# Performance work log

Measured on AMD Instinct MI355X. Metric: run time of the kernel, lower is better.

The kernel has to match this reference:

```python
import jax, jax.numpy as jnp
import numpy as np

B, T, C, H = 2, 2048, 1024, 16
HD = C // H  # 64


def setup_inputs() -> dict:
    key = jax.random.key(0)
    ks = jax.random.split(key, 5)
    x = jax.random.normal(ks[0], (B, T, C), jnp.float32)
    scale = 0.02
    Wq = jax.random.normal(ks[1], (C, C), jnp.float32) * scale
    Wk = jax.random.normal(ks[2], (C, C), jnp.float32) * scale
    Wv = jax.random.normal(ks[3], (C, C), jnp.float32) * scale
    Wo = jax.random.normal(ks[4], (C, C), jnp.float32) * scale
    # RoPE tables: freqs_cis = exp(i * pos * theta_j), theta_j = 10000^(-2j/HD)
    pos = jnp.arange(T, dtype=jnp.float32)
    theta = 10000.0 ** (-jnp.arange(0, HD, 2, dtype=jnp.float32) / HD)  # [HD/2]
    ang = pos[:, None] * theta[None, :]  # [T, HD/2]
    cos = jnp.cos(ang)
    sin = jnp.sin(ang)
    return {"x": x, "Wq": Wq, "Wk": Wk, "Wv": Wv, "Wo": Wo, "cos": cos, "sin": sin}


def _rope(t, cos, sin):
    # t: [B,T,H,HD]; pairs (even, odd) along last dim form complex numbers
    b, s, h, hd = t.shape
    tr = t.reshape(b, s, h, hd // 2, 2)
    t0, t1 = tr[..., 0], tr[..., 1]
    c = cos[None, :, None, :]  # [1,T,1,HD/2]
    sn = sin[None, :, None, :]
    o0 = t0 * c - t1 * sn
    o1 = t0 * sn + t1 * c
    return jnp.stack([o0, o1], axis=-1).reshape(b, s, h, hd)


def reference(x, Wq, Wk, Wv, Wo, cos, sin):
    b, t, c = x.shape
    h, hd = H, c // H
    q = (x @ Wq.T).reshape(b, t, h, hd)
    k = (x @ Wk.T).reshape(b, t, h, hd)
    v = (x @ Wv.T).reshape(b, t, h, hd)
    q = _rope(q, cos, sin)
    k = _rope(k, cos, sin)
    # explicit causal attention with full TxT score matrix (as in source)
    att = jnp.einsum("bthd,bshd->bhts", q, k) / jnp.sqrt(jnp.float32(hd))
    causal = jnp.tril(jnp.ones((t, t), dtype=bool))
    att = jnp.where(causal[None, None, :, :], att, -jnp.inf)
    att = jax.nn.softmax(att, axis=-1)
    out = jnp.einsum("bhts,bshd->bthd", att, v).reshape(b, t, c)
    return out @ Wo.T
```

## Files before the change

### kernel.cpp

```cpp
#include <hip/hip_runtime.h>
#include <cstdint>
#include <cstddef>


typedef __bf16 bf16;
typedef float  f32x4  __attribute__((ext_vector_type(4)));
typedef __bf16 bf16x4 __attribute__((ext_vector_type(4)));
typedef __bf16 bf16x8 __attribute__((ext_vector_type(8)));

constexpr int Bb = 2, Tt = 2048, Cc = 1024, Hh = 16;
constexpr int Mrows = Bb * Tt;
constexpr int NT = Tt / 64;
constexpr int LDS_ = 72;

#define GLOAD_LDS16(gp, lp)                                                      \
    __builtin_amdgcn_global_load_lds(                                            \
        (const __attribute__((address_space(1))) void*)(gp),                     \
        (__attribute__((address_space(3))) void*)(lp), 16, 0, 0)

#define QUAD_T(v0, v1, v2, v3, c2)                                               \
    {                                                                            \
        float e0 = (c2 & 1) ? v0 : v1, e1 = (c2 & 1) ? v2 : v3;                  \
        e0 = __shfl_xor(e0, 1); e1 = __shfl_xor(e1, 1);                          \
        if (c2 & 1) { v0 = e0; v2 = e1; } else { v1 = e0; v3 = e1; }             \
        float f0 = (c2 & 2) ? v0 : v2, f1 = (c2 & 2) ? v1 : v3;                  \
        f0 = __shfl_xor(f0, 2); f1 = __shfl_xor(f1, 2);                          \
        if (c2 & 2) { v0 = f0; v1 = f1; } else { v2 = f0; v3 = f1; }             \
    }

__global__ __launch_bounds__(256) void convert_k(const float* __restrict__ x,
                                                 const float* __restrict__ Wq,
                                                 const float* __restrict__ Wk,
                                                 const float* __restrict__ Wv,
                                                 const float* __restrict__ Wo,
                                                 const float* __restrict__ cosb,
                                                 const float* __restrict__ sinb,
                                                 bf16* __restrict__ xb,
                                                 bf16* __restrict__ Wqkv,
                                                 bf16* __restrict__ Wob,
                                                 float2* __restrict__ cs)
{
    if (blockIdx.x >= 4096) {
        int pi = ((blockIdx.x - 4096) * 256 + threadIdx.x) * 8;
#pragma unroll
        for (int u = 0; u < 8; ++u)
            cs[pi + u] = float2{cosb[pi + u], sinb[pi + u]};
        return;
    }
    uint32_t id = blockIdx.x * 256 + threadIdx.x;
    const float* src; bf16* dst; float sc = 1.0f;
    if (id < 524288u) {
        uint32_t tile = id >> 10, slot = id & 1023;
        uint32_t row = (tile >> 4) * 128 + (slot >> 9) * 64 +
                       ((slot >> 6) & 3) * 16 + (slot & 15);
        uint32_t k = (tile & 15) * 64 + ((slot >> 8) & 1) * 32 + ((slot >> 4) & 3) * 8;
        src = x + (size_t)row * 1024 + k;
        dst = xb + (size_t)id * 8;
    } else if (id < 917504u) {
        uint32_t t2 = id - 524288u;
        uint32_t tile = t2 >> 10, slot = t2 & 1023;
        uint32_t n = (tile >> 4) * 128 + (slot >> 9) * 64 +
                     ((slot >> 6) & 3) * 16 + (slot & 15);
        uint32_t k = (tile & 15) * 64 + ((slot >> 8) & 1) * 32 + ((slot >> 4) & 3) * 8;
        if (n < 1024)      { src = Wq + (size_t)n * 1024 + k;
                             sc = 0.125f * 1.44269504088896f; }
        else if (n < 2048)   src = Wk + (size_t)(n - 1024) * 1024 + k;
        else                 src = Wv + (size_t)(n - 2048) * 1024 + k;
        dst = Wqkv + (size_t)t2 * 8;
    } else {
        uint32_t t3 = id - 917504u;
        uint32_t tile = t3 >> 9, slot = t3 & 511;
        uint32_t n = (tile >> 4) * 64 + (slot >> 8) * 32 +
                     ((slot >> 6) & 1) * 16 + (slot & 15);
        uint32_t k = (tile & 15) * 64 + ((slot >> 7) & 1) * 32 + ((slot >> 4) & 3) * 8;
        src = Wo + (size_t)n * 1024 + k;
        dst = Wob + (size_t)t3 * 8;
    }
    float4 v0 = *(const float4*)(src);
    float4 v1 = *(const float4*)(src + 4);
    bf16x8 t;
    t[0] = (bf16)(v0.x*sc); t[1] = (bf16)(v0.y*sc); t[2] = (bf16)(v0.z*sc); t[3] = (bf16)(v0.w*sc);
    t[4] = (bf16)(v1.x*sc); t[5] = (bf16)(v1.y*sc); t[6] = (bf16)(v1.z*sc); t[7] = (bf16)(v1.w*sc);
    *(bf16x8*)dst = t;
}

__global__ __launch_bounds__(256) void gemm_qkv(const bf16* __restrict__ A,
                                                const bf16* __restrict__ W,
                                                bf16* __restrict__ QK,
                                                bf16* __restrict__ Vt,
                                                const float2* __restrict__ cs)
{
    __shared__ bf16 As[8192];
    __shared__ bf16 Ws[8192];
    const int tid  = threadIdx.x;
    const int lane = tid & 63, wave = tid >> 6;
    const int rhw = wave >> 1, chw = wave & 1;
    const int wr = rhw * 64, wc = chw * 64;
    const int l16 = lane & 15, lq = lane >> 4;
    const int row0 = blockIdx.x * 128, col0 = blockIdx.y * 128;

    f32x4 acc[4][4];
#pragma unroll
    for (int i = 0; i < 4; ++i)
#pragma unroll
        for (int j = 0; j < 4; ++j) acc[i][j] = f32x4{0.f, 0.f, 0.f, 0.f};

    const bf16* At = A + (size_t)blockIdx.x * 16 * 8192;
    const bf16* Wt = W + (size_t)blockIdx.y * 16 * 8192;

    for (int kb = 0; kb < 16; ++kb) {
        const bf16* at = At + kb * 8192;
        const bf16* wt = Wt + kb * 8192;
#pragma unroll
        for (int rnd = 0; rnd < 4; ++rnd) {
            const int seg = rnd * 4 + wave;
            GLOAD_LDS16(at + seg * 512 + lane * 8, &As[seg * 512]);
            GLOAD_LDS16(wt + seg * 512 + lane * 8, &Ws[seg * 512]);
        }
        __syncthreads();
#pragma unroll
        for (int ks = 0; ks < 2; ++ks) {
            bf16x8 af[4], bfr[4];
#pragma unroll
            for (int i = 0; i < 4; ++i)
                af[i] = *(const bf16x8*)(&As[(rhw * 512 + ks * 256 + i * 64 + lq * 16 + l16) * 8]);
#pragma unroll
            for (int j = 0; j < 4; ++j)
                bfr[j] = *(const bf16x8*)(&Ws[(chw * 512 + ks * 256 + j * 64 + lq * 16 + l16) * 8]);
#pragma unroll
            for (int i = 0; i < 4; ++i)
#pragma unroll
                for (int j = 0; j < 4; ++j)
                    acc[i][j] = __builtin_amdgcn_mfma_f32_16x16x32_bf16(
                        af[i], bfr[j], acc[i][j], 0, 0, 0);
        }
        __syncthreads();
    }

    const int c2 = l16 & 3, g4 = (l16 >> 2) * 4;
    if (blockIdx.y < 16) {
#pragma unroll
        for (int i = 0; i < 4; ++i)
#pragma unroll
            for (int j = 0; j < 4; ++j) {
                float v0 = acc[i][j][0], v1 = acc[i][j][1];
                float v2 = acc[i][j][2], v3 = acc[i][j][3];
                QUAD_T(v0, v1, v2, v3, c2);
                const int row = row0 + wr + i * 16 + lq * 4 + c2;
                const int t   = row & (Tt - 1);
                const int colb = wc + j * 16 + g4;
                const int p0   = (colb & 63) >> 1;
                float4 cp = *(const float4*)(&cs[t * 32 + p0]);
                bf16x4 pk;
                pk[0] = (bf16)(v0 * cp.x - v1 * cp.y);
                pk[1] = (bf16)(v0 * cp.y + v1 * cp.x);
                pk[2] = (bf16)(v2 * cp.z - v3 * cp.w);
                pk[3] = (bf16)(v2 * cp.w + v3 * cp.z);
                *(bf16x4*)(&QK[(size_t)row * 2048 + col0 + colb]) = pk;
            }
    } else {
#pragma unroll
        for (int i = 0; i < 4; ++i)
#pragma unroll
            for (int j = 0; j < 4; ++j) {
                const int dfull = col0 - 2048 + wc + j * 16 + l16;
                const int h = dfull >> 6, d = dfull & 63;
                const int row = row0 + wr + i * 16 + lq * 4;
                const int b = row >> 11, t = row & (Tt - 1);
                bf16x4 pk;
                pk[0] = (bf16)acc[i][j][0]; pk[1] = (bf16)acc[i][j][1];
                pk[2] = (bf16)acc[i][j][2]; pk[3] = (bf16)acc[i][j][3];
                *(bf16x4*)(&Vt[((size_t)(b * 16 + h) * 64 + d) * (size_t)Tt + t]) = pk;
            }
    }
}

__global__ __launch_bounds__(256) void gemm_o(const bf16* __restrict__ A,
                                              const bf16* __restrict__ W,
                                              float* __restrict__ Out)
{
    __shared__ bf16 As[8192];
    __shared__ bf16 Ws[4096];
    const int tid  = threadIdx.x;
    const int lane = tid & 63, wave = tid >> 6;
    const int rhw = wave >> 1, chw = wave & 1;
    const int wr = rhw * 64, wc = chw * 32;
    const int l16 = lane & 15, lq = lane >> 4;
    const int row0 = blockIdx.x * 128, col0 = blockIdx.y * 64;

    f32x4 acc[4][2];
#pragma unroll
    for (int i = 0; i < 4; ++i)
#pragma unroll
        for (int j = 0; j < 2; ++j) acc[i][j] = f32x4{0.f, 0.f, 0.f, 0.f};

    const bf16* At = A + (size_t)blockIdx.x * 16 * 8192;
    const bf16* Wt = W + (size_t)blockIdx.y * 16 * 4096;

    for (int kb = 0; kb < 16; ++kb) {
        const bf16* at = At + kb * 8192;
        const bf16* wt = Wt + kb * 4096;
#pragma unroll
        for (int rnd = 0; rnd < 4; ++rnd) {
            const int seg = rnd * 4 + wave;
            GLOAD_LDS16(at + seg * 512 + lane * 8, &As[seg * 512]);
        }
#pragma unroll
        for (int rnd = 0; rnd < 2; ++rnd) {
            const int seg = rnd * 4 + wave;
            GLOAD_LDS16(wt + seg * 512 + lane * 8, &Ws[seg * 512]);
        }
        __syncthreads();
#pragma unroll
        for (int ks = 0; ks < 2; ++ks) {
            bf16x8 af[4], bfr[2];
#pragma unroll
            for (int i = 0; i < 4; ++i)
                af[i] = *(const bf16x8*)(&As[(rhw * 512 + ks * 256 + i * 64 + lq * 16 + l16) * 8]);
#pragma unroll
            for (int j = 0; j < 2; ++j)
                bfr[j] = *(const bf16x8*)(&Ws[(chw * 256 + ks * 128 + j * 64 + lq * 16 + l16) * 8]);
#pragma unroll
            for (int i = 0; i < 4; ++i)
#pragma unroll
                for (int j = 0; j < 2; ++j)
                    acc[i][j] = __builtin_amdgcn_mfma_f32_16x16x32_bf16(
                        af[i], bfr[j], acc[i][j], 0, 0, 0);
        }
        __syncthreads();
    }
    const int c2 = l16 & 3, g4 = (l16 >> 2) * 4;
#pragma unroll
    for (int i = 0; i < 4; ++i)
#pragma unroll
        for (int j = 0; j < 2; ++j) {
            float v0 = acc[i][j][0], v1 = acc[i][j][1];
            float v2 = acc[i][j][2], v3 = acc[i][j][3];
            QUAD_T(v0, v1, v2, v3, c2);
            const int row = row0 + wr + i * 16 + lq * 4 + c2;
            const int col = col0 + wc + j * 16 + g4;
            *(float4*)(&Out[(size_t)row * Cc + col]) = float4{v0, v1, v2, v3};
        }
}

__global__ __launch_bounds__(256, 4) void attn_k(const bf16* __restrict__ QK,
                                                 const bf16* __restrict__ Vt,
                                                 bf16* __restrict__ O)
{
    __shared__ bf16 Ks[64 * LDS_];
    __shared__ bf16 Vs[64 * LDS_];
    const int tid = threadIdx.x;
    const int wv = tid >> 6, lane = tid & 63;
    const int l16 = lane & 15, lq = lane >> 4;
    const int bh = blockIdx.y, b = bh >> 4, h = bh & 15;
    const int kr = tid >> 2, c0 = (tid & 3) * 16;
    const int pr = 32 * (kr >> 5) + 16 * ((kr >> 2) & 1) + 4 * ((kr >> 3) & 3) + (kr & 3);

    const bf16* kcol = QK + 1024 + (size_t)(b * Tt + kr) * 2048 + h * 64 + c0;
    const bf16* vcol = Vt + ((size_t)bh * 64 + kr) * Tt + c0;

    for (int phase = 0; phase < 2; ++phase) {
        const int qt = phase ? blockIdx.x : (NT - 1 - blockIdx.x);

        const int qglob = qt * 64 + wv * 16 + l16;
        const bf16* qp = QK + (size_t)(b * Tt + qglob) * 2048 + h * 64;
        bf16x8 qf0 = *(const bf16x8*)(qp + lq * 8);
        bf16x8 qf1 = *(const bf16x8*)(qp + 32 + lq * 8);

        uint4 pk0 = *(const uint4*)(kcol);
        uint4 pk1 = *(const uint4*)(kcol + 8);
        uint4 pv0 = *(const uint4*)(vcol);
        uint4 pv1 = *(const uint4*)(vcol + 8);

        float l = 0.f;
        f32x4 o[4];
#pragma unroll
        for (int dt = 0; dt < 4; ++dt) o[dt] = f32x4{0.f, 0.f, 0.f, 0.f};

        for (int t = 0; t <= qt; ++t) {
            *(uint4*)(&Ks[pr * LDS_ + c0])     = pk0;
            *(uint4*)(&Ks[pr * LDS_ + c0 + 8]) = pk1;
            *(uint4*)(&Vs[kr * LDS_ + c0])     = pv0;
            *(uint4*)(&Vs[kr * LDS_ + c0 + 8]) = pv1;
            __syncthreads();
            if (t < qt) {
                const bf16* kn = kcol + (size_t)(t + 1) * 64 * 2048;
                const bf16* vn = vcol + (t + 1) * 64;
                pk0 = *(const uint4*)(kn);
                pk1 = *(const uint4*)(kn + 8);
                pv0 = *(const uint4*)(vn);
                pv1 = *(const uint4*)(vn + 8);
            }

            f32x4 s[4];
#pragma unroll
            for (int mt = 0; mt < 4; ++mt) s[mt] = f32x4{0.f, 0.f, 0.f, 0.f};
#pragma unroll
            for (int mt = 0; mt < 4; ++mt) {
                bf16x8 a0 = *(const bf16x8*)(&Ks[(mt * 16 + l16) * LDS_ + lq * 8]);
                s[mt] = __builtin_amdgcn_mfma_f32_16x16x32_bf16(a0, qf0, s[mt], 0, 0, 0);
            }
#pragma unroll
            for (int mt = 0; mt < 4; ++mt) {
                bf16x8 a1 = *(const bf16x8*)(&Ks[(mt * 16 + l16) * LDS_ + 32 + lq * 8]);
                s[mt] = __builtin_amdgcn_mfma_f32_16x16x32_bf16(a1, qf1, s[mt], 0, 0, 0);
            }
            if (t == qt) {
                const int qloc = wv * 16 + l16;
#pragma unroll
                for (int mt = 0; mt < 4; ++mt)
#pragma unroll
                    for (int r = 0; r < 4; ++r) {
                        int keyl = (mt >> 1) * 32 + lq * 8 + (mt & 1) * 4 + r;
                        if (keyl > qloc) s[mt][r] = -1e30f;
                    }
            }
            bf16x8 pb0, pb1;
#pragma unroll
            for (int mt = 0; mt < 4; ++mt)
#pragma unroll
                for (int r = 0; r < 4; ++r) {
                    float p = exp2f(s[mt][r]);
                    l += p;
                    s[mt][r] = p;
                }
#pragma unroll
            for (int r = 0; r < 4; ++r) {
                pb0[r]     = (bf16)s[0][r];
                pb0[4 + r] = (bf16)s[1][r];
                pb1[r]     = (bf16)s[2][r];
                pb1[4 + r] = (bf16)s[3][r];
            }
#pragma unroll
            for (int dt = 0; dt < 4; ++dt) {
                bf16x8 v0 = *(const bf16x8*)(&Vs[(dt * 16 + l16) * LDS_ + lq * 8]);
                o[dt] = __builtin_amdgcn_mfma_f32_16x16x32_bf16(v0, pb0, o[dt], 0, 0, 0);
            }
#pragma unroll
            for (int dt = 0; dt < 4; ++dt) {
                bf16x8 v1 = *(const bf16x8*)(&Vs[(dt * 16 + l16) * LDS_ + 32 + lq * 8]);
                o[dt] = __builtin_amdgcn_mfma_f32_16x16x32_bf16(v1, pb1, o[dt], 0, 0, 0);
            }
            __syncthreads();
        }
        l += __shfl_xor(l, 16);
        l += __shfl_xor(l, 32);
        float inv = 1.f / l;
        bf16* obase = O + ((size_t)(b * 16 + (qt >> 1)) * 16 + h) * 8192;
        const int rh = qt & 1;
#pragma unroll
        for (int dt = 0; dt < 4; ++dt) {
            bf16x4 pk;
#pragma unroll
            for (int r = 0; r < 4; ++r) pk[r] = (bf16)(o[dt][r] * inv);
            const int slot = rh * 512 + (dt >> 1) * 256 + wv * 64 +
                             ((dt & 1) * 2 + (lq >> 1)) * 16 + l16;
            *(bf16x4*)(obase + slot * 8 + (lq & 1) * 4) = pk;
        }
    }
}

extern "C" void kernel_launch(void* const* d_in, const int* in_sizes, int n_in,
                              void* d_out, int out_size, void* d_ws, size_t ws_size,
                              hipStream_t stream)
{
    const float* x    = (const float*)d_in[0];
    const float* Wq   = (const float*)d_in[1];
    const float* Wk   = (const float*)d_in[2];
    const float* Wv   = (const float*)d_in[3];
    const float* Wo   = (const float*)d_in[4];
    const float* cosb = (const float*)d_in[5];
    const float* sinb = (const float*)d_in[6];

    constexpr size_t M1 = 1024 * 1024;
    bf16* base = (bf16*)d_ws;
    bf16*   xb   = base;
    bf16*   QK   = base + 4 * M1;
    bf16*   VtG  = base + 12 * M1;
    bf16*   Wqkv = base + 16 * M1;
    bf16*   Wob  = base + 19 * M1;
    float2* csT  = (float2*)(base + 20 * M1);
    bf16*   Ow   = xb;

    convert_k<<<4096 + 32, 256, 0, stream>>>(x, Wq, Wk, Wv, Wo, cosb, sinb,
                                             xb, Wqkv, Wob, csT);

    gemm_qkv<<<dim3(Mrows / 128, 3072 / 128), 256, 0, stream>>>(
        xb, Wqkv, QK, VtG, csT);

    attn_k<<<dim3(NT / 2, Bb * Hh), 256, 0, stream>>>(QK, VtG, Ow);

    gemm_o<<<dim3(Mrows / 128, Cc / 64), 256, 0, stream>>>(Ow, Wob, (float*)d_out);
}
```

Before: 174.6 us.

## Double-buffer K/V tiles in LDS and remap attention blocks for locality

```diff
diff --git a/kernel.cpp b/kernel.cpp
--- a/kernel.cpp
+++ b/kernel.cpp
@@ -247,12 +247,15 @@
                                                  const bf16* __restrict__ Vt,
                                                  bf16* __restrict__ O)
 {
-    __shared__ bf16 Ks[64 * LDS_];
-    __shared__ bf16 Vs[64 * LDS_];
+    __shared__ bf16 Ks[2][64 * LDS_];
+    __shared__ bf16 Vs[2][64 * LDS_];
     const int tid = threadIdx.x;
     const int wv = tid >> 6, lane = tid & 63;
     const int l16 = lane & 15, lq = lane >> 4;
-    const int bh = blockIdx.y, b = bh >> 4, h = bh & 15;
+    const int id = blockIdx.y * 16 + blockIdx.x;
+    const int bh = (id & 7) * 4 + (id >> 7);
+    const int pi = (id >> 3) & 15;
+    const int b = bh >> 4, h = bh & 15;
     const int kr = tid >> 2, c0 = (tid & 3) * 16;
     const int pr = 32 * (kr >> 5) + 16 * ((kr >> 2) & 1) + 4 * ((kr >> 3) & 3) + (kr & 3);
 
@@ -260,7 +263,7 @@
     const bf16* vcol = Vt + ((size_t)bh * 64 + kr) * Tt + c0;
 
     for (int phase = 0; phase < 2; ++phase) {
-        const int qt = phase ? blockIdx.x : (NT - 1 - blockIdx.x);
+        const int qt = phase ? pi : (NT - 1 - pi);
 
         const int qglob = qt * 64 + wv * 16 + l16;
         const bf16* qp = QK + (size_t)(b * Tt + qglob) * 2048 + h * 64;
@@ -271,6 +274,11 @@
         uint4 pk1 = *(const uint4*)(kcol + 8);
         uint4 pv0 = *(const uint4*)(vcol);
         uint4 pv1 = *(const uint4*)(vcol + 8);
+        *(uint4*)(&Ks[0][pr * LDS_ + c0])     = pk0;
+        *(uint4*)(&Ks[0][pr * LDS_ + c0 + 8]) = pk1;
+        *(uint4*)(&Vs[0][kr * LDS_ + c0])     = pv0;
+        *(uint4*)(&Vs[0][kr * LDS_ + c0 + 8]) = pv1;
+        __syncthreads();
 
         float l = 0.f;
         f32x4 o[4];
@@ -278,11 +286,7 @@
         for (int dt = 0; dt < 4; ++dt) o[dt] = f32x4{0.f, 0.f, 0.f, 0.f};
 
         for (int t = 0; t <= qt; ++t) {
-            *(uint4*)(&Ks[pr * LDS_ + c0])     = pk0;
-            *(uint4*)(&Ks[pr * LDS_ + c0 + 8]) = pk1;
-            *(uint4*)(&Vs[kr * LDS_ + c0])     = pv0;
-            *(uint4*)(&Vs[kr * LDS_ + c0 + 8]) = pv1;
-            __syncthreads();
+            const int cur = t & 1;
             if (t < qt) {
                 const bf16* kn = kcol + (size_t)(t + 1) * 64 * 2048;
                 const bf16* vn = vcol + (t + 1) * 64;
@@ -297,12 +301,12 @@
             for (int mt = 0; mt < 4; ++mt) s[mt] = f32x4{0.f, 0.f, 0.f, 0.f};
 #pragma unroll
             for (int mt = 0; mt < 4; ++mt) {
-                bf16x8 a0 = *(const bf16x8*)(&Ks[(mt * 16 + l16) * LDS_ + lq * 8]);
+                bf16x8 a0 = *(const bf16x8*)(&Ks[cur][(mt * 16 + l16) * LDS_ + lq * 8]);
                 s[mt] = __builtin_amdgcn_mfma_f32_16x16x32_bf16(a0, qf0, s[mt], 0, 0, 0);
             }
 #pragma unroll
             for (int mt = 0; mt < 4; ++mt) {
-                bf16x8 a1 = *(const bf16x8*)(&Ks[(mt * 16 + l16) * LDS_ + 32 + lq * 8]);
+                bf16x8 a1 = *(const bf16x8*)(&Ks[cur][(mt * 16 + l16) * LDS_ + 32 + lq * 8]);
                 s[mt] = __builtin_amdgcn_mfma_f32_16x16x32_bf16(a1, qf1, s[mt], 0, 0, 0);
             }
             if (t == qt) {
@@ -333,13 +337,19 @@
             }
 #pragma unroll
             for (int dt = 0; dt < 4; ++dt) {
-                bf16x8 v0 = *(const bf16x8*)(&Vs[(dt * 16 + l16) * LDS_ + lq * 8]);
+                bf16x8 v0 = *(const bf16x8*)(&Vs[cur][(dt * 16 + l16) * LDS_ + lq * 8]);
                 o[dt] = __builtin_amdgcn_mfma_f32_16x16x32_bf16(v0, pb0, o[dt], 0, 0, 0);
             }
 #pragma unroll
             for (int dt = 0; dt < 4; ++dt) {
-                bf16x8 v1 = *(const bf16x8*)(&Vs[(dt * 16 + l16) * LDS_ + 32 + lq * 8]);
+                bf16x8 v1 = *(const bf16x8*)(&Vs[cur][(dt * 16 + l16) * LDS_ + 32 + lq * 8]);
                 o[dt] = __builtin_amdgcn_mfma_f32_16x16x32_bf16(v1, pb1, o[dt], 0, 0, 0);
+            }
+            if (t < qt) {
+                *(uint4*)(&Ks[cur ^ 1][pr * LDS_ + c0])     = pk0;
+                *(uint4*)(&Ks[cur ^ 1][pr * LDS_ + c0 + 8]) = pk1;
+                *(uint4*)(&Vs[cur ^ 1][kr * LDS_ + c0])     = pv0;
+                *(uint4*)(&Vs[cur ^ 1][kr * LDS_ + c0 + 8]) = pv1;
             }
             __syncthreads();
         }
```

After: 172.5 us. Within noise of the previous version (-1.2%).
